# Kernel tuning notes

Hardware: AMD Instinct MI355X
Metric: run time of the kernel (lower is better)

The kernel has to match this reference:

```python
import jax, jax.numpy as jnp
import numpy as np
import math

D = 2048
N_HEADS = 16
D_HEAD = D // N_HEADS
B = 2
L = 2048


def _rope_tables(seq_len, d_head, base=10000.0):
    # standard half-rotation RoPE tables, shape [L, d_head]
    inv_freq = 1.0 / (base ** (jnp.arange(0, d_head, 2, dtype=jnp.float32) / d_head))
    ang = jnp.arange(seq_len, dtype=jnp.float32)[:, None] * inv_freq[None, :]  # [L, d_head/2]
    cos = jnp.concatenate([jnp.cos(ang), jnp.cos(ang)], axis=-1)  # [L, d_head]
    sin = jnp.concatenate([jnp.sin(ang), jnp.sin(ang)], axis=-1)
    return cos, sin


def _apply_rope(x, cos, sin):
    # x: [B, H, L, d_head]; rotate_half convention
    half = x.shape[-1] // 2
    x_rot = jnp.concatenate([-x[..., half:], x[..., :half]], axis=-1)
    return x * cos[None, None, :, :] + x_rot * sin[None, None, :, :]


def setup_inputs() -> dict:
    key = jax.random.key(0)
    k1, k2, k3 = jax.random.split(key, 3)
    x = jax.random.normal(k1, (B, L, D), dtype=jnp.float32)
    w_qkv = jax.random.normal(k2, (D, 3 * D), dtype=jnp.float32) * (1.0 / math.sqrt(D))
    w_out = jax.random.normal(k3, (D, D), dtype=jnp.float32) * (1.0 / math.sqrt(D))
    s_qk = jnp.asarray(math.sqrt(D_HEAD), dtype=jnp.float32)  # init sqrt(d_head)
    return {"x": x, "w_qkv": w_qkv, "w_out": w_out, "s_qk": s_qk}


def reference(x, w_qkv, w_out, s_qk):
    Bs, Ls, Ds = x.shape
    qkv = jnp.einsum("bld,de->ble", x, w_qkv).reshape(Bs, Ls, 3, N_HEADS, D_HEAD)
    q, k, v = qkv[:, :, 0], qkv[:, :, 1], qkv[:, :, 2]
    # -> [B, H, L, d_head]
    q = jnp.transpose(q, (0, 2, 1, 3))
    k = jnp.transpose(k, (0, 2, 1, 3))
    v = jnp.transpose(v, (0, 2, 1, 3))
    cos, sin = _rope_tables(Ls, D_HEAD)
    q = _apply_rope(q, cos, sin)
    k = _apply_rope(k, cos, sin)
    # L2-normalize per head (torch F.normalize eps=1e-12)
    q = q / jnp.maximum(jnp.linalg.norm(q, axis=-1, keepdims=True), 1e-12)
    k = k / jnp.maximum(jnp.linalg.norm(k, axis=-1, keepdims=True), 1e-12)
    # softmax((q*s_qk) @ k^T) with causal mask, scale=1.0
    scores = jnp.einsum("bhqd,bhkd->bhqk", q * s_qk, k)
    causal = jnp.tril(jnp.ones((Ls, Ls), dtype=bool))
    scores = jnp.where(causal[None, None, :, :], scores, -jnp.inf)
    attn = jax.nn.softmax(scores, axis=-1)
    out = jnp.einsum("bhqk,bhkd->bhqd", attn, v)
    out = jnp.transpose(out, (0, 2, 1, 3)).reshape(Bs, Ls, Ds)
    return jnp.einsum("bld,de->ble", out, w_out)
```

## Files before the change

kernel.cpp:

```cpp
#include <hip/hip_runtime.h>
#include <math.h>


#define D 2048
#define NH 16
#define DH 128
#define BB 2
#define LL 2048
#define BHD (BB*NH)
#define MROWS (BB*LL)
#define KDIM D

typedef __attribute__((ext_vector_type(8))) short short8;
typedef __attribute__((ext_vector_type(4))) float floatx4;

__device__ __forceinline__ unsigned short f2bf(float f) {
    unsigned u = __float_as_uint(f);
    unsigned r = u + 0x7FFFu + ((u >> 16) & 1u);
    return (unsigned short)(r >> 16);
}
__device__ __forceinline__ float bf2f(unsigned short u) {
    return __uint_as_float(((unsigned)u) << 16);
}

__device__ __forceinline__ void async16(const void* g, void* lds) {
    __builtin_amdgcn_global_load_lds(
        (const __attribute__((address_space(1))) unsigned int*)g,
        (__attribute__((address_space(3))) unsigned int*)lds, 16, 0, 0);
}

template<int CTRL>
__device__ __forceinline__ float dpp_movf(float x) {
    return __int_as_float(__builtin_amdgcn_update_dpp(
        0, __float_as_int(x), CTRL, 0xF, 0xF, true));
}
__device__ __forceinline__ float row_max16(float x) {
    x = fmaxf(x, dpp_movf<0xB1>(x));
    x = fmaxf(x, dpp_movf<0x4E>(x));
    x = fmaxf(x, dpp_movf<0x124>(x));
    x = fmaxf(x, dpp_movf<0x128>(x));
    return x;
}
__device__ __forceinline__ float row_sum16(float x) {
    x += dpp_movf<0xB1>(x);
    x += dpp_movf<0x4E>(x);
    x += dpp_movf<0x124>(x);
    x += dpp_movf<0x128>(x);
    return x;
}

__global__ __launch_bounds__(256)
void cast_bf16_r15(const float* __restrict__ in,
                   unsigned short* __restrict__ out, int n4)
{
    int i = blockIdx.x * 256 + threadIdx.x;
    if (i < n4) {
        float4 v = ((const float4*)in)[i];
        ushort4 o;
        o.x = f2bf(v.x); o.y = f2bf(v.y); o.z = f2bf(v.z); o.w = f2bf(v.w);
        ((ushort4*)out)[i] = o;
    }
}

__global__ __launch_bounds__(256)
void transpose_cast_r15(const float* __restrict__ W,
                        unsigned short* __restrict__ Wt, int K, int N)
{
    __shared__ float tile[32][33];
    const int tx = threadIdx.x & 31, ty = threadIdx.x >> 5;
    const int n0 = blockIdx.x * 32, k0 = blockIdx.y * 32;
#pragma unroll
    for (int r = 0; r < 4; r++)
        tile[ty + 8 * r][tx] = W[(size_t)(k0 + ty + 8 * r) * N + n0 + tx];
    __syncthreads();
#pragma unroll
    for (int r = 0; r < 4; r++)
        Wt[(size_t)(n0 + ty + 8 * r) * K + k0 + tx] = f2bf(tile[tx][ty + 8 * r]);
}

template<int N, int MODE>
__global__ __launch_bounds__(256)
void gemm_mfma_r15(const unsigned short* __restrict__ A,
                   const unsigned short* __restrict__ Bt,
                   float* __restrict__ C, unsigned short* __restrict__ Qo,
                   unsigned short* __restrict__ Ko, unsigned short* __restrict__ Vo)
{
    __shared__ unsigned short As[128 * 32];
    __shared__ unsigned short Bs[128 * 32];
    const int t = threadIdx.x;
    const int w = t >> 6, lane = t & 63;
    const int lrow = lane & 15, quad = lane >> 4;

    const int lin = blockIdx.y * gridDim.x + blockIdx.x;
    const int xcd = lin & 7, idx = lin >> 3;
    const int m0 = (xcd * 4 + (idx & 3)) * 128;
    const int n0 = (idx >> 2) * 128;

    const int wm = (w >> 1) * 64, wn = (w & 1) * 64;

    floatx4 acc[4][4];
#pragma unroll
    for (int i = 0; i < 4; i++)
#pragma unroll
        for (int j = 0; j < 4; j++) acc[i][j] = (floatx4){0.f, 0.f, 0.f, 0.f};

    const int srow = 32 * w + (lane >> 2);
    const int sseg = (lane & 3) * 8;

    for (int k0 = 0; k0 < KDIM; k0 += 32) {
        __syncthreads();
        async16(&A [(size_t)(m0 + srow)      * KDIM + k0 + sseg], &As[(32 * w)      * 32]);
        async16(&A [(size_t)(m0 + srow + 16) * KDIM + k0 + sseg], &As[(32 * w + 16) * 32]);
        async16(&Bt[(size_t)(n0 + srow)      * KDIM + k0 + sseg], &Bs[(32 * w)      * 32]);
        async16(&Bt[(size_t)(n0 + srow + 16) * KDIM + k0 + sseg], &Bs[(32 * w + 16) * 32]);
        __syncthreads();

        short8 a[4], b[4];
#pragma unroll
        for (int i = 0; i < 4; i++)
            a[i] = *(const short8*)&As[(wm + i * 16 + lrow) * 32 + quad * 8];
#pragma unroll
        for (int j = 0; j < 4; j++)
            b[j] = *(const short8*)&Bs[(wn + j * 16 + lrow) * 32 + quad * 8];
#pragma unroll
        for (int i = 0; i < 4; i++)
#pragma unroll
            for (int j = 0; j < 4; j++)
                acc[i][j] = __builtin_amdgcn_mfma_f32_16x16x32_bf16(a[i], b[j], acc[i][j], 0, 0, 0);
    }

    if (MODE == 0) {
#pragma unroll
        for (int i = 0; i < 4; i++)
#pragma unroll
            for (int j = 0; j < 4; j++) {
                int col = n0 + wn + j * 16 + lrow;
#pragma unroll
                for (int r = 0; r < 4; r++) {
                    int m = m0 + wm + i * 16 + quad * 4 + r;
                    C[(size_t)m * N + col] = acc[i][j][r];
                }
            }
    } else {
        const int s = n0 >> 11;
        const int h = (n0 & 2047) >> 7;
        if (s == 2) {
#pragma unroll
            for (int i = 0; i < 4; i++) {
                int m = m0 + wm + i * 16 + quad * 4;
                int b = m >> 11, l = m & 2047;
#pragma unroll
                for (int j = 0; j < 4; j++) {
                    int dh = wn + j * 16 + lrow;
                    ushort4 v;
                    v.x = f2bf(acc[i][j][0]); v.y = f2bf(acc[i][j][1]);
                    v.z = f2bf(acc[i][j][2]); v.w = f2bf(acc[i][j][3]);
                    *(ushort4*)&Vo[(((size_t)b * NH + h) * DH + dh) * LL + l] = v;
                }
            }
        } else {
            unsigned short* dst = (s == 0) ? Qo : Ko;
#pragma unroll
            for (int i = 0; i < 4; i++)
#pragma unroll
                for (int j = 0; j < 4; j++) {
                    int dh = wn + j * 16 + lrow;
#pragma unroll
                    for (int r = 0; r < 4; r++) {
                        int m = m0 + wm + i * 16 + quad * 4 + r;
                        int b = m >> 11, l = m & 2047;
                        dst[(((size_t)b * NH + h) * LL + l) * DH + dh] = f2bf(acc[i][j][r]);
                    }
                }
        }
    }
}

__global__ __launch_bounds__(256)
void rope_norm_r15(unsigned short* __restrict__ Q,
                   unsigned short* __restrict__ K,
                   const float* __restrict__ s_qk_ptr)
{
    const int wid  = threadIdx.x >> 6;
    const int lane = threadIdx.x & 63;
    const int row  = blockIdx.x * 4 + wid;
    const int l    = row & (LL - 1);
    const size_t base = (size_t)row * DH;

    float ang = (float)l * expf(-0.14391157f * (float)lane);
    float c = cosf(ang), s = sinf(ang);

    float qlo = bf2f(Q[base + lane]), qhi = bf2f(Q[base + lane + 64]);
    float klo = bf2f(K[base + lane]), khi = bf2f(K[base + lane + 64]);

    float qr_lo = fmaf(qlo, c, (-qhi) * s);
    float qr_hi = fmaf(qhi, c,   qlo  * s);
    float kr_lo = fmaf(klo, c, (-khi) * s);
    float kr_hi = fmaf(khi, c,   klo  * s);

    float qs = qr_lo * qr_lo + qr_hi * qr_hi;
    float ks = kr_lo * kr_lo + kr_hi * kr_hi;
    qs = row_sum16(qs);  ks = row_sum16(ks);
    qs += __shfl_xor(qs, 16);  ks += __shfl_xor(ks, 16);
    qs += __shfl_xor(qs, 32);  ks += __shfl_xor(ks, 32);
    float qn = fmaxf(sqrtf(qs), 1e-12f);
    float kn = fmaxf(sqrtf(ks), 1e-12f);

    float sqk = s_qk_ptr[0];
    Q[base + lane]      = f2bf(qr_lo / qn * sqk);
    Q[base + lane + 64] = f2bf(qr_hi / qn * sqk);
    K[base + lane]      = f2bf(kr_lo / kn);
    K[base + lane + 64] = f2bf(kr_hi / kn);
}

#define ABQ 128
#define ABK 64
__global__ __launch_bounds__(256, 2)
void attn_mfma_r15(const unsigned short* __restrict__ Q,
                   const unsigned short* __restrict__ K,
                   const unsigned short* __restrict__ Vt,
                   unsigned short* __restrict__ AOb)
{
    __shared__ __align__(16) unsigned short Ks[2][ABK * DH];
    __shared__ __align__(16) unsigned short Vs[2][DH * ABK];
    __shared__ __align__(16) unsigned short Ps[4][32][64];

    const int t = threadIdx.x;
    const int w = t >> 6, lane = t & 63;
    const int lrow = lane & 15, quad = lane >> 4;
    const int bh = blockIdx.x;
    const int y  = blockIdx.y;
    const int qt = (y < 8) ? (15 - y) : (y - 8);
    const int q0 = qt * ABQ;
    const int qw = q0 + w * 32;

    const unsigned short* Qb = Q  + (size_t)bh * LL * DH;
    const unsigned short* Kb = K  + (size_t)bh * LL * DH;
    const unsigned short* Vg = Vt + (size_t)bh * DH * LL;

    short8 aq[2][4];
#pragma unroll
    for (int h = 0; h < 2; h++)
#pragma unroll
        for (int kk = 0; kk < 4; kk++)
            aq[h][kk] = *(const short8*)&Qb[(size_t)(qw + 16 * h + lrow) * DH
                                            + kk * 32 + quad * 8];

    floatx4 oacc[2][8];
#pragma unroll
    for (int h = 0; h < 2; h++)
#pragma unroll
        for (int dt = 0; dt < 8; dt++) oacc[h][dt] = (floatx4){0.f, 0.f, 0.f, 0.f};
    float mrow[2][4], lsum[2][4];
#pragma unroll
    for (int h = 0; h < 2; h++)
#pragma unroll
        for (int r = 0; r < 4; r++) { mrow[h][r] = -1e30f; lsum[h][r] = 0.f; }

    auto STAGE = [&](int tile, int buf) {
        const int k0s = tile * ABK;
#pragma unroll
        for (int c = 0; c < 4; c++) {
            int row = 16 * w + 4 * c;
            int r   = row + (lane >> 4);
            int col = (lane & 15) ^ (r & 7);
            async16(&Kb[(size_t)(k0s + r) * DH + col * 8], &Ks[buf][row * DH]);
        }
#pragma unroll
        for (int c = 0; c < 4; c++) {
            int row = 32 * w + 8 * c;
            int r   = row + (lane >> 3);
            int col = (lane & 7) ^ (r & 7);
            async16(&Vg[(size_t)r * LL + k0s + col * 8], &Vs[buf][row * ABK]);
        }
    };

    const int ntiles = 2 * qt + 2;
    STAGE(0, 0);
    __syncthreads();

    int cur = 0;
    for (int tile = 0; tile < ntiles; tile++) {
        const int k0 = tile * ABK;
        if (tile + 1 < ntiles) STAGE(tile + 1, cur ^ 1);

        floatx4 sacc[2][4];
#pragma unroll
        for (int h = 0; h < 2; h++)
#pragma unroll
            for (int j = 0; j < 4; j++) sacc[h][j] = (floatx4){0.f, 0.f, 0.f, 0.f};
        __builtin_amdgcn_s_setprio(1);
#pragma unroll
        for (int kk = 0; kk < 4; kk++) {
#pragma unroll
            for (int j = 0; j < 4; j++) {
                int slot = (kk * 4 + quad) ^ (lrow & 7);
                short8 bk = *(const short8*)&Ks[cur][(j * 16 + lrow) * DH + slot * 8];
                sacc[0][j] = __builtin_amdgcn_mfma_f32_16x16x32_bf16(aq[0][kk], bk, sacc[0][j], 0, 0, 0);
                sacc[1][j] = __builtin_amdgcn_mfma_f32_16x16x32_bf16(aq[1][kk], bk, sacc[1][j], 0, 0, 0);
            }
        }
        __builtin_amdgcn_s_setprio(0);

#pragma unroll
        for (int h = 0; h < 2; h++) {
            if (k0 + ABK - 1 > qw + 16 * h) {
#pragma unroll
                for (int j = 0; j < 4; j++) {
                    int key = k0 + j * 16 + lrow;
#pragma unroll
                    for (int r = 0; r < 4; r++) {
                        int q = qw + 16 * h + quad * 4 + r;
                        if (key > q) sacc[h][j][r] = -1e30f;
                    }
                }
            }
        }

        float mt_[2][4];
#pragma unroll
        for (int h = 0; h < 2; h++)
#pragma unroll
            for (int r = 0; r < 4; r++) {
                float mt = fmaxf(fmaxf(sacc[h][0][r], sacc[h][1][r]),
                                 fmaxf(sacc[h][2][r], sacc[h][3][r]));
                mt_[h][r] = row_max16(mt);
            }
        bool defer = true;
#pragma unroll
        for (int h = 0; h < 2; h++)
#pragma unroll
            for (int r = 0; r < 4; r++)
                defer = defer && (mt_[h][r] - mrow[h][r] <= 8.0f);
        defer = __all(defer);

        float alpha[2][4];
        if (!defer) {
#pragma unroll
            for (int h = 0; h < 2; h++)
#pragma unroll
                for (int r = 0; r < 4; r++) {
                    float mn = fmaxf(mrow[h][r], mt_[h][r]);
                    alpha[h][r] = __expf(mrow[h][r] - mn);
                    mrow[h][r] = mn;
                }
        }

#pragma unroll
        for (int r = 0; r < 4; r++) {
            const int rp0 = quad * 4 + r;
            const int rowp = (lane & 1) ? (16 + rp0) : rp0;
            float rs0 = 0.f, rs1 = 0.f;
#pragma unroll
            for (int j = 0; j < 4; j++) {
                float p0 = __expf(sacc[0][j][r] - mrow[0][r]);
                float p1 = __expf(sacc[1][j][r] - mrow[1][r]);
                rs0 += p0; rs1 += p1;
                float n0 = dpp_movf<0xB1>(p0);
                float n1 = dpp_movf<0xB1>(p1);
                unsigned pk = (lane & 1)
                    ? ((unsigned)f2bf(n1) | ((unsigned)f2bf(p1) << 16))
                    : ((unsigned)f2bf(p0) | ((unsigned)f2bf(n0) << 16));
                int slot = (2 * j + (lrow >> 3)) ^ (rp0 & 7);
                *(unsigned*)&Ps[w][rowp][slot * 8 + (lrow & 6)] = pk;
            }
            rs0 = row_sum16(rs0); rs1 = row_sum16(rs1);
            if (defer) {
                lsum[0][r] += rs0;
                lsum[1][r] += rs1;
            } else {
                lsum[0][r] = lsum[0][r] * alpha[0][r] + rs0;
                lsum[1][r] = lsum[1][r] * alpha[1][r] + rs1;
            }
        }
        if (!defer) {
#pragma unroll
            for (int h = 0; h < 2; h++)
#pragma unroll
                for (int dt = 0; dt < 8; dt++)
#pragma unroll
                    for (int r = 0; r < 4; r++) oacc[h][dt][r] *= alpha[h][r];
        }

        __builtin_amdgcn_s_setprio(1);
#pragma unroll
        for (int kk2 = 0; kk2 < 2; kk2++) {
            int pslot = (kk2 * 4 + quad) ^ (lrow & 7);
            short8 pa0 = *(const short8*)&Ps[w][lrow][pslot * 8];
            short8 pa1 = *(const short8*)&Ps[w][16 + lrow][pslot * 8];
#pragma unroll
            for (int dt = 0; dt < 8; dt++) {
                int slot = (kk2 * 4 + quad) ^ (lrow & 7);
                short8 bv = *(const short8*)&Vs[cur][(dt * 16 + lrow) * ABK + slot * 8];
                oacc[0][dt] = __builtin_amdgcn_mfma_f32_16x16x32_bf16(pa0, bv, oacc[0][dt], 0, 0, 0);
                oacc[1][dt] = __builtin_amdgcn_mfma_f32_16x16x32_bf16(pa1, bv, oacc[1][dt], 0, 0, 0);
            }
        }
        __builtin_amdgcn_s_setprio(0);

        __syncthreads();
        cur ^= 1;
    }

    const int b = bh >> 4, hd = bh & 15;
#pragma unroll
    for (int h = 0; h < 2; h++)
#pragma unroll
        for (int r = 0; r < 4; r++) {
            float inv = 1.f / lsum[h][r];
            int q = qw + 16 * h + quad * 4 + r;
            size_t base = ((size_t)b * LL + q) * D + hd * DH;
#pragma unroll
            for (int dt = 0; dt < 8; dt++)
                AOb[base + dt * 16 + lrow] = f2bf(oacc[h][dt][r] * inv);
        }
}

extern "C" void kernel_launch(void* const* d_in, const int* in_sizes, int n_in,
                              void* d_out, int out_size, void* d_ws, size_t ws_size,
                              hipStream_t stream)
{
    const float* x     = (const float*)d_in[0];
    const float* w_qkv = (const float*)d_in[1];
    const float* w_out = (const float*)d_in[2];
    const float* s_qk  = (const float*)d_in[3];
    float* out = (float*)d_out;

    const size_t SZ = (size_t)BB * NH * LL * DH;
    unsigned short* u = (unsigned short*)d_ws;
    unsigned short* xb    = u;
    unsigned short* wqkvT = xb    + (size_t)MROWS * KDIM;
    unsigned short* woutT = wqkvT + (size_t)(3 * D) * KDIM;
    unsigned short* Qb    = woutT + (size_t)D * KDIM;
    unsigned short* Kb    = Qb + SZ;
    unsigned short* VtG   = Kb + SZ;

    cast_bf16_r15<<<(MROWS * KDIM / 4 + 255) / 256, 256, 0, stream>>>(
        x, xb, MROWS * KDIM / 4);
    transpose_cast_r15<<<dim3(3 * D / 32, KDIM / 32), 256, 0, stream>>>(
        w_qkv, wqkvT, KDIM, 3 * D);
    gemm_mfma_r15<3 * D, 1><<<dim3(3 * D / 128, MROWS / 128), 256, 0, stream>>>(
        xb, wqkvT, nullptr, Qb, Kb, VtG);
    rope_norm_r15<<<dim3(BHD * LL / 4), 256, 0, stream>>>(Qb, Kb, s_qk);
    attn_mfma_r15<<<dim3(BHD, LL / ABQ), 256, 0, stream>>>(Qb, Kb, VtG, xb);
    transpose_cast_r15<<<dim3(D / 32, D / 32), 256, 0, stream>>>(
        w_out, woutT, D, D);
    gemm_mfma_r15<D, 0><<<dim3(D / 128, MROWS / 128), 256, 0, stream>>>(
        xb, woutT, out, nullptr, nullptr, nullptr);
}
```

Measured before the change: 454.0 us.

## Write V row-major from QKV GEMM, transpose in separate kernel, drop XCD swizzle

```diff
diff --git a/kernel.cpp b/kernel.cpp
--- a/kernel.cpp
+++ b/kernel.cpp
@@ -50,7 +50,7 @@
 }
 
 __global__ __launch_bounds__(256)
-void cast_bf16_r15(const float* __restrict__ in,
+void cast_bf16_r16(const float* __restrict__ in,
                    unsigned short* __restrict__ out, int n4)
 {
     int i = blockIdx.x * 256 + threadIdx.x;
@@ -63,7 +63,7 @@
 }
 
 __global__ __launch_bounds__(256)
-void transpose_cast_r15(const float* __restrict__ W,
+void transpose_cast_r16(const float* __restrict__ W,
                         unsigned short* __restrict__ Wt, int K, int N)
 {
     __shared__ float tile[32][33];
@@ -78,9 +78,28 @@
         Wt[(size_t)(n0 + ty + 8 * r) * K + k0 + tx] = f2bf(tile[tx][ty + 8 * r]);
 }
 
+__global__ __launch_bounds__(256)
+void transpose_v_r16(const unsigned short* __restrict__ Vb,
+                     unsigned short* __restrict__ VtG)
+{
+    __shared__ unsigned short tile[32][34];
+    const int tx = threadIdx.x & 31, ty = threadIdx.x >> 5;
+    const int l0 = blockIdx.x * 32, d0 = blockIdx.y * 32;
+    const int bh = blockIdx.z;
+    const unsigned short* src = Vb + (size_t)bh * LL * DH;
+    unsigned short* dst = VtG + (size_t)bh * DH * LL;
+#pragma unroll
+    for (int r = 0; r < 4; r++)
+        tile[ty + 8 * r][tx] = src[(size_t)(l0 + ty + 8 * r) * DH + d0 + tx];
+    __syncthreads();
+#pragma unroll
+    for (int r = 0; r < 4; r++)
+        dst[(size_t)(d0 + ty + 8 * r) * LL + l0 + tx] = tile[tx][ty + 8 * r];
+}
+
 template<int N, int MODE>
 __global__ __launch_bounds__(256)
-void gemm_mfma_r15(const unsigned short* __restrict__ A,
+void gemm_mfma_r16(const unsigned short* __restrict__ A,
                    const unsigned short* __restrict__ Bt,
                    float* __restrict__ C, unsigned short* __restrict__ Qo,
                    unsigned short* __restrict__ Ko, unsigned short* __restrict__ Vo)
@@ -90,12 +109,7 @@
     const int t = threadIdx.x;
     const int w = t >> 6, lane = t & 63;
     const int lrow = lane & 15, quad = lane >> 4;
-
-    const int lin = blockIdx.y * gridDim.x + blockIdx.x;
-    const int xcd = lin & 7, idx = lin >> 3;
-    const int m0 = (xcd * 4 + (idx & 3)) * 128;
-    const int n0 = (idx >> 2) * 128;
-
+    const int m0 = blockIdx.y * 128, n0 = blockIdx.x * 128;
     const int wm = (w >> 1) * 64, wn = (w & 1) * 64;
 
     floatx4 acc[4][4];
@@ -144,40 +158,24 @@
     } else {
         const int s = n0 >> 11;
         const int h = (n0 & 2047) >> 7;
-        if (s == 2) {
-#pragma unroll
-            for (int i = 0; i < 4; i++) {
-                int m = m0 + wm + i * 16 + quad * 4;
-                int b = m >> 11, l = m & 2047;
-#pragma unroll
-                for (int j = 0; j < 4; j++) {
-                    int dh = wn + j * 16 + lrow;
-                    ushort4 v;
-                    v.x = f2bf(acc[i][j][0]); v.y = f2bf(acc[i][j][1]);
-                    v.z = f2bf(acc[i][j][2]); v.w = f2bf(acc[i][j][3]);
-                    *(ushort4*)&Vo[(((size_t)b * NH + h) * DH + dh) * LL + l] = v;
+        unsigned short* dst = (s == 0) ? Qo : (s == 1) ? Ko : Vo;
+#pragma unroll
+        for (int i = 0; i < 4; i++)
+#pragma unroll
+            for (int j = 0; j < 4; j++) {
+                int dh = wn + j * 16 + lrow;
+#pragma unroll
+                for (int r = 0; r < 4; r++) {
+                    int m = m0 + wm + i * 16 + quad * 4 + r;
+                    int b = m >> 11, l = m & 2047;
+                    dst[(((size_t)b * NH + h) * LL + l) * DH + dh] = f2bf(acc[i][j][r]);
                 }
             }
-        } else {
-            unsigned short* dst = (s == 0) ? Qo : Ko;
-#pragma unroll
-            for (int i = 0; i < 4; i++)
-#pragma unroll
-                for (int j = 0; j < 4; j++) {
-                    int dh = wn + j * 16 + lrow;
-#pragma unroll
-                    for (int r = 0; r < 4; r++) {
-                        int m = m0 + wm + i * 16 + quad * 4 + r;
-                        int b = m >> 11, l = m & 2047;
-                        dst[(((size_t)b * NH + h) * LL + l) * DH + dh] = f2bf(acc[i][j][r]);
-                    }
-                }
-        }
     }
 }
 
 __global__ __launch_bounds__(256)
-void rope_norm_r15(unsigned short* __restrict__ Q,
+void rope_norm_r16(unsigned short* __restrict__ Q,
                    unsigned short* __restrict__ K,
                    const float* __restrict__ s_qk_ptr)
 {
@@ -216,7 +214,7 @@
 #define ABQ 128
 #define ABK 64
 __global__ __launch_bounds__(256, 2)
-void attn_mfma_r15(const unsigned short* __restrict__ Q,
+void attn_mfma_r16(const unsigned short* __restrict__ Q,
                    const unsigned short* __restrict__ K,
                    const unsigned short* __restrict__ Vt,
                    unsigned short* __restrict__ AOb)
@@ -433,18 +431,20 @@
     unsigned short* woutT = wqkvT + (size_t)(3 * D) * KDIM;
     unsigned short* Qb    = woutT + (size_t)D * KDIM;
     unsigned short* Kb    = Qb + SZ;
-    unsigned short* VtG   = Kb + SZ;
-
-    cast_bf16_r15<<<(MROWS * KDIM / 4 + 255) / 256, 256, 0, stream>>>(
+    unsigned short* Vb    = Kb + SZ;
+    unsigned short* VtG   = Vb + SZ;
+
+    cast_bf16_r16<<<(MROWS * KDIM / 4 + 255) / 256, 256, 0, stream>>>(
         x, xb, MROWS * KDIM / 4);
-    transpose_cast_r15<<<dim3(3 * D / 32, KDIM / 32), 256, 0, stream>>>(
+    transpose_cast_r16<<<dim3(3 * D / 32, KDIM / 32), 256, 0, stream>>>(
         w_qkv, wqkvT, KDIM, 3 * D);
-    gemm_mfma_r15<3 * D, 1><<<dim3(3 * D / 128, MROWS / 128), 256, 0, stream>>>(
-        xb, wqkvT, nullptr, Qb, Kb, VtG);
-    rope_norm_r15<<<dim3(BHD * LL / 4), 256, 0, stream>>>(Qb, Kb, s_qk);
-    attn_mfma_r15<<<dim3(BHD, LL / ABQ), 256, 0, stream>>>(Qb, Kb, VtG, xb);
-    transpose_cast_r15<<<dim3(D / 32, D / 32), 256, 0, stream>>>(
+    gemm_mfma_r16<3 * D, 1><<<dim3(3 * D / 128, MROWS / 128), 256, 0, stream>>>(
+        xb, wqkvT, nullptr, Qb, Kb, Vb);
+    rope_norm_r16<<<dim3(BHD * LL / 4), 256, 0, stream>>>(Qb, Kb, s_qk);
+    transpose_v_r16<<<dim3(LL / 32, DH / 32, BHD), 256, 0, stream>>>(Vb, VtG);
+    attn_mfma_r16<<<dim3(BHD, LL / ABQ), 256, 0, stream>>>(Qb, Kb, VtG, xb);
+    transpose_cast_r16<<<dim3(D / 32, D / 32), 256, 0, stream>>>(
         w_out, woutT, D, D);
-    gemm_mfma_r15<D, 0><<<dim3(D / 128, MROWS / 128), 256, 0, stream>>>(
+    gemm_mfma_r16<D, 0><<<dim3(D / 128, MROWS / 128), 256, 0, stream>>>(
         xb, woutT, out, nullptr, nullptr, nullptr);
 }
```

Measured after the change: 429.1 us. 1.06x faster.
